# Kernel optimization log

Hardware: AMD Instinct MI355X
Metric: run time of the kernel (lower is better)

## Reference

```python
import jax, jax.numpy as jnp
import numpy as np

N_RBF = 20
CUTOFF = 5.0
N_BASIS = 128
N_FILTERS = 128
N_LAYERS = 3
B, N = 128, 128
N_PAIRS = 524288


def ssp(x):
    # ShiftedSoftplus: softplus(x) - log(2)
    return jax.nn.softplus(x) - jnp.log(2.0).astype(x.dtype)


def gaussian_rbf(d):
    # schnetpack-style GaussianRBF: offsets in [0, cutoff], shared width
    offsets = jnp.linspace(0.0, CUTOFF, N_RBF, dtype=d.dtype)
    width = offsets[1] - offsets[0]
    coeff = -0.5 / (width * width)
    diff = d[:, None] - offsets[None, :]  # [n_pairs, n_rbf]
    return jnp.exp(coeff * diff * diff)


def cosine_cutoff(d):
    fc = 0.5 * (jnp.cos(d * (jnp.pi / CUTOFF)) + 1.0)
    return fc * (d < CUTOFF).astype(d.dtype)


def setup_inputs() -> dict:
    key = jax.random.key(0)
    ks = jax.random.split(key, 16)
    inp = {
        "Z": jax.random.randint(ks[0], (B, N), 0, 100),
        "R": jax.random.normal(ks[1], (B, N, 3), dtype=jnp.float32) * 2.0,
        "idx_i": jax.random.randint(ks[2], (N_PAIRS,), 0, B * N),
        "idx_j": jax.random.randint(ks[3], (N_PAIRS,), 0, B * N),
        "emb": jax.random.normal(ks[4], (100, N_BASIS), dtype=jnp.float32) * 0.1,
    }
    s = 0.05
    inp["in2f_W"] = jax.random.normal(ks[5], (N_LAYERS, N_BASIS, N_FILTERS), dtype=jnp.float32) * s
    inp["in2f_b"] = jnp.zeros((N_LAYERS, N_FILTERS), dtype=jnp.float32)
    inp["fW1"] = jax.random.normal(ks[6], (N_LAYERS, N_RBF, N_FILTERS), dtype=jnp.float32) * s
    inp["fb1"] = jnp.zeros((N_LAYERS, N_FILTERS), dtype=jnp.float32)
    inp["fW2"] = jax.random.normal(ks[7], (N_LAYERS, N_FILTERS, N_FILTERS), dtype=jnp.float32) * s
    inp["fb2"] = jnp.zeros((N_LAYERS, N_FILTERS), dtype=jnp.float32)
    inp["oW1"] = jax.random.normal(ks[8], (N_LAYERS, N_FILTERS, N_BASIS), dtype=jnp.float32) * s
    inp["ob1"] = jnp.zeros((N_LAYERS, N_BASIS), dtype=jnp.float32)
    inp["oW2"] = jax.random.normal(ks[9], (N_LAYERS, N_BASIS, N_BASIS), dtype=jnp.float32) * s
    inp["ob2"] = jnp.zeros((N_LAYERS, N_BASIS), dtype=jnp.float32)
    return inp


def _interaction(x, f_ij, rcut_ij, idx_i, idx_j, W_in, b_in, fW1, fb1, fW2, fb2, oW1, ob1, oW2, ob2):
    # x: [B, N, n_atom_basis]
    h = jnp.einsum("bnf,fg->bng", x, W_in) + b_in          # input_to_feature
    h = h.reshape(-1, h.shape[-1])                           # [B*N, n_filters]
    # filter network on RBFs
    Wij = ssp(f_ij @ fW1 + fb1) @ fW2 + fb2                  # [n_pairs, n_filters]
    Wij = Wij * rcut_ij[:, None]
    x_ij = h[idx_j] * Wij                                     # gather + multiply
    agg = jax.ops.segment_sum(x_ij, idx_i, num_segments=h.shape[0])  # scatter_add
    out = ssp(agg @ oW1 + ob1) @ oW2 + ob2                    # feature_to_output
    return out.reshape(x.shape[0], x.shape[1], N_BASIS)


def reference(Z, R, idx_i, idx_j, emb, in2f_W, in2f_b, fW1, fb1, fW2, fb2, oW1, ob1, oW2, ob2):
    coords = R.reshape(-1, 3)                                 # [B*N, 3]
    vec = coords[idx_i] - coords[idx_j]
    d_ij = jnp.linalg.norm(vec, axis=-1)                      # [n_pairs]
    f_ij = gaussian_rbf(d_ij)                                 # [n_pairs, 20]
    rcut_ij = cosine_cutoff(d_ij)                             # [n_pairs]
    x = emb[Z]                                                # [B, N, 128]
    for l in range(N_LAYERS):
        v = _interaction(x, f_ij, rcut_ij, idx_i, idx_j,
                         in2f_W[l], in2f_b[l], fW1[l], fb1[l], fW2[l], fb2[l],
                         oW1[l], ob1[l], oW2[l], ob2[l])
        x = x + v
    return x
```

## Files before the change

kernel.cpp:

```cpp
#include <hip/hip_runtime.h>
#include <hip/hip_fp16.h>

#define NPAIRS 524288
#define NATOMS 16384
#define TBINS  2048
#define TROWS  2049
#define CAP    80
#define CUTOFF_F 5.0f

#define MB_G0    256
#define MB_TAB   (MB_G0 + 771)
#define MB_WC    (MB_TAB + 72)
#define MB_TOTAL (MB_WC + 2048)

typedef _Float16 f16;
typedef f16 f16x4 __attribute__((ext_vector_type(4)));
typedef f16 f16x8 __attribute__((ext_vector_type(8)));
typedef float f32x4 __attribute__((ext_vector_type(4)));

__device__ __forceinline__ float sspf(float v) {
  float a = fabsf(v);
  return fmaxf(v, 0.0f) + log1pf(expf(-a)) - 0.69314718055994531f;
}

__device__ __forceinline__ int swz(int row, int kh) {
  return (row << 8) + ((kh << 1) ^ ((row & 7) << 4));
}
__device__ __forceinline__ int swzW(int col, int kh) {
  return (col << 7) + ((kh << 1) ^ ((col & 7) << 4));
}
__device__ __forceinline__ f16x8 ldW(const f16* __restrict__ Wg, int col, int ss, int hi) {
  return *(const f16x8*)((const char*)Wg + (ss >> 1) * 16384 + swzW(col, (ss & 1) * 32 + hi * 8));
}

__device__ __forceinline__ uint4 ld16(const char* __restrict__ base, int byteOff) {
  return *(const uint4*)(base + byteOff);
}
__device__ __forceinline__ void dot8(float* acc, uint4 wv, uint4 hv) {
  const __half* wp = (const __half*)&wv;
  const __half* hp = (const __half*)&hv;
  #pragma unroll
  for (int q = 0; q < 8; ++q)
    acc[q] = fmaf(__half2float(wp[q]), __half2float(hp[q]), acc[q]);
}

__global__ __launch_bounds__(256) void zero_kernel(int* __restrict__ p) {
  p[blockIdx.x * 256 + threadIdx.x] = 0;
}

__global__ __launch_bounds__(256) void mega(const int* __restrict__ Z,
                                            const float* __restrict__ emb,
                                            const float* __restrict__ in2f_W,
                                            const float* __restrict__ in2f_b,
                                            const float* __restrict__ fW1,
                                            const float* __restrict__ fb1,
                                            const float* __restrict__ fW2,
                                            const float* __restrict__ fb2,
                                            const float* __restrict__ oW1,
                                            const float* __restrict__ oW2,
                                            const int* __restrict__ idx_i,
                                            const int* __restrict__ idx_j,
                                            const float* __restrict__ R,
                                            f16* __restrict__ table,
                                            f16* __restrict__ wsw,
                                            int* __restrict__ cursor,
                                            int2* __restrict__ pjd,
                                            f16* __restrict__ hout) {
  __shared__ char smem[16384];
  int t = threadIdx.x;
  int bid = blockIdx.x;

  if (bid < MB_G0) {
    char* Wl = smem;
    size_t rbase = (size_t)bid * 64;
    int w = t >> 6, lane = t & 63;
    int lo = lane & 15, hi = lane >> 4;

    int z = Z[rbase + 16 * w + lo];
    const float* erow = emb + (size_t)z * 128;
    f16x8 fa[4];
    #pragma unroll
    for (int ss = 0; ss < 4; ++ss) {
      float4 a = *(const float4*)(erow + ss * 32 + hi * 8);
      float4 b = *(const float4*)(erow + ss * 32 + hi * 8 + 4);
      f16x8 v = { (f16)a.x, (f16)a.y, (f16)a.z, (f16)a.w,
                  (f16)b.x, (f16)b.y, (f16)b.z, (f16)b.w };
      fa[ss] = v;
    }

    f32x4 acc[8];
    #pragma unroll
    for (int cb = 0; cb < 8; ++cb) acc[cb] = (f32x4){0.0f, 0.0f, 0.0f, 0.0f};

    #pragma unroll
    for (int h = 0; h < 2; ++h) {
      #pragma unroll
      for (int i = 0; i < 4; ++i) {
        int tloc = i * 256 + t;
        int col = tloc & 127, kc = tloc >> 7;
        f16x8 v;
        #pragma unroll
        for (int kk = 0; kk < 8; ++kk)
          v[kk] = (f16)in2f_W[(h * 64 + kc * 8 + kk) * 128 + col];
        *(f16x8*)(Wl + swzW(col, kc * 8)) = v;
      }
      __syncthreads();
      #pragma unroll
      for (int cb = 0; cb < 8; ++cb) {
        int col = cb * 16 + lo;
        #pragma unroll
        for (int sh = 0; sh < 2; ++sh) {
          f16x8 fb = *(f16x8*)(Wl + swzW(col, sh * 32 + hi * 8));
          acc[cb] = __builtin_amdgcn_mfma_f32_16x16x32_f16(fa[h * 2 + sh], fb, acc[cb], 0, 0, 0);
        }
      }
      __syncthreads();
    }

    #pragma unroll
    for (int cb = 0; cb < 8; ++cb) {
      int col = cb * 16 + lo;
      float bc = in2f_b[col];
      #pragma unroll
      for (int j = 0; j < 4; ++j)
        hout[(rbase + 16 * w + hi * 4 + j) * 128 + col] = (f16)(acc[cb][j] + bc);
    }
    return;
  }

  if (bid < MB_TAB) {
    float* hid = (float*)smem;
    int bid2 = bid - MB_G0;
    int l = bid2 / 257, rem = bid2 % 257;
    int e = t >> 5, q = t & 31;
    int ti = rem * 8 + e;
    const float* W1 = fW1 + (size_t)l * 20 * 128;
    const float* B1 = fb1 + (size_t)l * 128;
    const float* W2 = fW2 + (size_t)l * 128 * 128;
    const float* B2 = fb2 + (size_t)l * 128;

    const float width = CUTOFF_F / 19.0f;
    const float coeff = -0.5f / (width * width);
    const float dstep = CUTOFF_F / (float)TBINS;
    float d = (float)ti * dstep;

    float4 h4 = *(const float4*)&B1[q * 4];
    #pragma unroll
    for (int r = 0; r < 20; ++r) {
      float diff = d - (float)r * width;
      float fr = expf(coeff * diff * diff);
      float4 w4 = *(const float4*)&W1[r * 128 + q * 4];
      h4.x += fr * w4.x; h4.y += fr * w4.y; h4.z += fr * w4.z; h4.w += fr * w4.w;
    }
    *(float4*)&hid[e * 128 + q * 4] =
        make_float4(sspf(h4.x), sspf(h4.y), sspf(h4.z), sspf(h4.w));
    __syncthreads();

    float4 o4 = *(const float4*)&B2[q * 4];
    const float4* W2g = (const float4*)W2;
    #pragma unroll 4
    for (int g = 0; g < 128; ++g) {
      float hv = hid[e * 128 + g];
      float4 w4 = W2g[g * 32 + q];
      o4.x += hv * w4.x; o4.y += hv * w4.y; o4.z += hv * w4.z; o4.w += hv * w4.w;
    }

    if (ti < TROWS) {
      float fc = (d < CUTOFF_F) ? 0.5f * (cosf(d * 0.62831853071795865f) + 1.0f) : 0.0f;
      f16x4 hv = { (f16)(o4.x * fc), (f16)(o4.y * fc), (f16)(o4.z * fc), (f16)(o4.w * fc) };
      *(f16x4*)((f16*)table + ((size_t)l * TROWS + ti) * 128 + q * 4) = hv;
    }
    return;
  }

  if (bid < MB_WC) {
    int bid2 = bid - MB_TAB;
    int mm = bid2 >> 3;
    int tloc = (bid2 & 7) * 256 + t;
    int col = tloc & 127, k0 = (tloc >> 7) << 3;
    const float* src = mm < 3 ? in2f_W + (size_t)mm * 16384
                     : mm < 6 ? oW1 + (size_t)(mm - 3) * 16384
                              : oW2 + (size_t)(mm - 6) * 16384;
    f16x8 v;
    #pragma unroll
    for (int kk = 0; kk < 8; ++kk) v[kk] = (f16)src[(k0 + kk) * 128 + col];
    *(f16x8*)((char*)wsw + (size_t)mm * 32768 + (k0 >> 6) * 16384 + swzW(col, k0 & 63)) = v;
    return;
  }

  {
    int p = (bid - MB_WC) * 256 + t;
    int i = idx_i[p], j = idx_j[p];
    float dx = R[(size_t)i*3+0] - R[(size_t)j*3+0];
    float dy = R[(size_t)i*3+1] - R[(size_t)j*3+1];
    float dz = R[(size_t)i*3+2] - R[(size_t)j*3+2];
    float d = sqrtf(dx*dx + dy*dy + dz*dz);
    if (d < CUTOFF_F) {
      int bin = __float2int_rn(d * ((float)TBINS / CUTOFF_F));
      int slot = atomicAdd(&cursor[i], 1);
      if (slot < CAP) pjd[i * CAP + slot] = make_int2(j << 8, bin << 8);
    }
  }
}

template <int FIRST, int HAS_NEXT>
__global__ __launch_bounds__(512, 4) void aggfuse(const int2* __restrict__ pjd,
                                                  const int* __restrict__ cnt,
                                                  const f16* __restrict__ hin,
                                                  const f16* __restrict__ tabL,
                                                  const f16* __restrict__ W1g,
                                                  const float* __restrict__ ob1,
                                                  const f16* __restrict__ W2g,
                                                  const float* __restrict__ ob2,
                                                  const int* __restrict__ Z,
                                                  const float* __restrict__ emb,
                                                  float* __restrict__ x,
                                                  const f16* __restrict__ Wng,
                                                  const float* __restrict__ bn,
                                                  f16* __restrict__ hout) {
  __shared__ char smem[8192];
  char* AlT = smem;
  char* Tl  = smem + 4096;
  int tid = threadIdx.x;
  int wv = tid >> 6, lane = tid & 63;
  int s = lane >> 4, c = lane & 15;
  int rbase = blockIdx.x * 16;

  {
    int a = rbase + wv * 2 + (s & 1);
    int half = s >> 1;
    const int2* pp = pjd + a * CAP;
    int n = min(cnt[a], CAP);
    int nh = half * 2;
    const char* hinB = (const char*)hin;
    const char* tabB = (const char*)tabL;
    int cb16 = c << 4;

    int m = (n + 3) >> 2;
    m = max(m, __shfl_xor(m, 16, 64));
    m = max(m, __shfl_xor(m, 32, 64));

    float acc[8];
    #pragma unroll
    for (int q = 0; q < 8; ++q) acc[q] = 0.0f;
    const int2 S2 = make_int2(0, TBINS << 8);

    int2 vA  = (nh     < n) ? pp[nh]     : S2;
    int2 vB  = (nh + 1 < n) ? pp[nh + 1] : S2;
    int2 vA1 = (nh + 4 < n) ? pp[nh + 4] : S2;
    int2 vB1 = (nh + 5 < n) ? pp[nh + 5] : S2;
    uint4 wA = ld16(tabB, vA.y + cb16), hA = ld16(hinB, vA.x + cb16);
    uint4 wB = ld16(tabB, vB.y + cb16), hB = ld16(hinB, vB.x + cb16);

    for (int it = 0; it < m; ++it) {
      int k2 = 4 * (it + 2) + nh;
      int2 vA2 = (k2 < n)     ? pp[k2]     : S2;
      int2 vB2 = (k2 + 1 < n) ? pp[k2 + 1] : S2;
      uint4 wAn = ld16(tabB, vA1.y + cb16), hAn = ld16(hinB, vA1.x + cb16);
      uint4 wBn = ld16(tabB, vB1.y + cb16), hBn = ld16(hinB, vB1.x + cb16);
      dot8(acc, wA, hA);
      dot8(acc, wB, hB);
      wA = wAn; hA = hAn; wB = wBn; hB = hBn;
      vA1 = vA2; vB1 = vB2;
    }

    #pragma unroll
    for (int q = 0; q < 8; ++q) acc[q] += __shfl_xor(acc[q], 32, 64);

    if (s < 2) {
      int row = wv * 2 + s;
      f16x8 pk;
      #pragma unroll
      for (int q = 0; q < 8; ++q) pk[q] = (f16)acc[q];
      *(f16x8*)(AlT + swz(row, c * 8)) = pk;
    }
  }
  __syncthreads();

  int lo = c, hi = s;
  int col = wv * 16 + lo;

  float res[4];
  if (FIRST) {
    #pragma unroll
    for (int j = 0; j < 4; ++j) {
      int z = Z[rbase + hi * 4 + j];
      res[j] = emb[(size_t)z * 128 + col];
    }
  } else {
    #pragma unroll
    for (int j = 0; j < 4; ++j)
      res[j] = x[(size_t)(rbase + hi * 4 + j) * 128 + col];
  }

  {
    f32x4 acc = {0.0f, 0.0f, 0.0f, 0.0f};
    #pragma unroll
    for (int ss = 0; ss < 4; ++ss) {
      f16x8 fa = *(f16x8*)(AlT + swz(lo, ss * 32 + hi * 8));
      acc = __builtin_amdgcn_mfma_f32_16x16x32_f16(fa, ldW(W1g, col, ss, hi), acc, 0, 0, 0);
    }
    float bc = ob1[col];
    #pragma unroll
    for (int j = 0; j < 4; ++j)
      *(f16*)(Tl + swz(hi * 4 + j, col)) = (f16)sspf(acc[j] + bc);
  }
  __syncthreads();

  {
    f32x4 acc = {0.0f, 0.0f, 0.0f, 0.0f};
    #pragma unroll
    for (int ss = 0; ss < 4; ++ss) {
      f16x8 fa = *(f16x8*)(Tl + swz(lo, ss * 32 + hi * 8));
      acc = __builtin_amdgcn_mfma_f32_16x16x32_f16(fa, ldW(W2g, col, ss, hi), acc, 0, 0, 0);
    }
    float bc = ob2[col];
    #pragma unroll
    for (int j = 0; j < 4; ++j) {
      int r = hi * 4 + j;
      float xn = res[j] + acc[j] + bc;
      x[(size_t)(rbase + r) * 128 + col] = xn;
      if (HAS_NEXT) *(f16*)(AlT + swz(r, col)) = (f16)xn;
    }
  }

  if (HAS_NEXT) {
    __syncthreads();
    f32x4 acc = {0.0f, 0.0f, 0.0f, 0.0f};
    #pragma unroll
    for (int ss = 0; ss < 4; ++ss) {
      f16x8 fa = *(f16x8*)(AlT + swz(lo, ss * 32 + hi * 8));
      acc = __builtin_amdgcn_mfma_f32_16x16x32_f16(fa, ldW(Wng, col, ss, hi), acc, 0, 0, 0);
    }
    float bc = bn[col];
    #pragma unroll
    for (int j = 0; j < 4; ++j)
      hout[(size_t)(rbase + hi * 4 + j) * 128 + col] = (f16)(acc[j] + bc);
  }
}

extern "C" void kernel_launch(void* const* d_in, const int* in_sizes, int n_in,
                              void* d_out, int out_size, void* d_ws, size_t ws_size,
                              hipStream_t stream) {
  const int*   Z      = (const int*)d_in[0];
  const float* R      = (const float*)d_in[1];
  const int*   idx_i  = (const int*)d_in[2];
  const int*   idx_j  = (const int*)d_in[3];
  const float* emb    = (const float*)d_in[4];
  const float* in2f_W = (const float*)d_in[5];
  const float* in2f_b = (const float*)d_in[6];
  const float* fW1    = (const float*)d_in[7];
  const float* fb1    = (const float*)d_in[8];
  const float* fW2    = (const float*)d_in[9];
  const float* fb2    = (const float*)d_in[10];
  const float* oW1    = (const float*)d_in[11];
  const float* ob1    = (const float*)d_in[12];
  const float* oW2    = (const float*)d_in[13];
  const float* ob2    = (const float*)d_in[14];
  float* x = (float*)d_out;

  char* ws = (char*)d_ws;
  int*  cursor = (int*) (ws + 0x0000000);
  int2* pjd    = (int2*)(ws + 0x0010000);
  f16*  table  = (f16*) (ws + 0x0B00000);
  f16*  h0     = (f16*) (ws + 0x0D00000);
  f16*  h1     = (f16*) (ws + 0x1100000);
  f16*  wsw    = (f16*) (ws + 0x1500000);

  zero_kernel<<<NATOMS / 256, 256, 0, stream>>>(cursor);
  mega<<<MB_TOTAL, 256, 0, stream>>>(Z, emb, in2f_W, in2f_b, fW1, fb1, fW2, fb2,
                                     oW1, oW2, idx_i, idx_j, R,
                                     table, wsw, cursor, pjd, h0);

  aggfuse<1, 1><<<NATOMS / 16, 512, 0, stream>>>(pjd, cursor, h0, table + 0 * (size_t)TROWS * 128,
                                                 wsw + 3 * 16384, ob1,
                                                 wsw + 6 * 16384, ob2,
                                                 Z, emb, x,
                                                 wsw + 1 * 16384, in2f_b + 128, h1);
  aggfuse<0, 1><<<NATOMS / 16, 512, 0, stream>>>(pjd, cursor, h1, table + 1 * (size_t)TROWS * 128,
                                                 wsw + 4 * 16384, ob1 + 128,
                                                 wsw + 7 * 16384, ob2 + 128,
                                                 Z, emb, x,
                                                 wsw + 2 * 16384, in2f_b + 256, h0);
  aggfuse<0, 0><<<NATOMS / 16, 512, 0, stream>>>(pjd, cursor, h0, table + 2 * (size_t)TROWS * 128,
                                                 wsw + 5 * 16384, ob1 + 256,
                                                 wsw + 8 * 16384, ob2 + 256,
                                                 Z, emb, x, nullptr, nullptr, nullptr);
}
```

Before: 116.4 us.

## Fuse three layer kernels into one persistent kernel with grid barriers

```diff
diff --git a/kernel.cpp b/kernel.cpp
--- a/kernel.cpp
+++ b/kernel.cpp
@@ -7,6 +7,7 @@
 #define TROWS  2049
 #define CAP    80
 #define CUTOFF_F 5.0f
+#define NBLK   512
 
 #define MB_G0    256
 #define MB_TAB   (MB_G0 + 771)
@@ -44,8 +45,10 @@
     acc[q] = fmaf(__half2float(wp[q]), __half2float(hp[q]), acc[q]);
 }
 
-__global__ __launch_bounds__(256) void zero_kernel(int* __restrict__ p) {
-  p[blockIdx.x * 256 + threadIdx.x] = 0;
+__global__ __launch_bounds__(256) void zero_kernel(int* __restrict__ cursor,
+                                                   int* __restrict__ barr) {
+  if (blockIdx.x < NATOMS / 256) cursor[blockIdx.x * 256 + threadIdx.x] = 0;
+  else barr[threadIdx.x] = 0;
 }
 
 __global__ __launch_bounds__(256) void mega(const int* __restrict__ Z,
@@ -203,85 +206,71 @@
   }
 }
 
-template <int FIRST, int HAS_NEXT>
-__global__ __launch_bounds__(512, 4) void aggfuse(const int2* __restrict__ pjd,
-                                                  const int* __restrict__ cnt,
-                                                  const f16* __restrict__ hin,
-                                                  const f16* __restrict__ tabL,
-                                                  const f16* __restrict__ W1g,
-                                                  const float* __restrict__ ob1,
-                                                  const f16* __restrict__ W2g,
-                                                  const float* __restrict__ ob2,
-                                                  const int* __restrict__ Z,
-                                                  const float* __restrict__ emb,
-                                                  float* __restrict__ x,
-                                                  const f16* __restrict__ Wng,
-                                                  const float* __restrict__ bn,
-                                                  f16* __restrict__ hout) {
-  __shared__ char smem[8192];
-  char* AlT = smem;
-  char* Tl  = smem + 4096;
-  int tid = threadIdx.x;
-  int wv = tid >> 6, lane = tid & 63;
-  int s = lane >> 4, c = lane & 15;
-  int rbase = blockIdx.x * 16;
-
-  {
-    int a = rbase + wv * 2 + (s & 1);
-    int half = s >> 1;
-    const int2* pp = pjd + a * CAP;
-    int n = min(cnt[a], CAP);
-    int nh = half * 2;
-    const char* hinB = (const char*)hin;
-    const char* tabB = (const char*)tabL;
-    int cb16 = c << 4;
-
-    int m = (n + 3) >> 2;
-    m = max(m, __shfl_xor(m, 16, 64));
-    m = max(m, __shfl_xor(m, 32, 64));
-
-    float acc[8];
-    #pragma unroll
-    for (int q = 0; q < 8; ++q) acc[q] = 0.0f;
-    const int2 S2 = make_int2(0, TBINS << 8);
-
-    int2 vA  = (nh     < n) ? pp[nh]     : S2;
-    int2 vB  = (nh + 1 < n) ? pp[nh + 1] : S2;
-    int2 vA1 = (nh + 4 < n) ? pp[nh + 4] : S2;
-    int2 vB1 = (nh + 5 < n) ? pp[nh + 5] : S2;
-    uint4 wA = ld16(tabB, vA.y + cb16), hA = ld16(hinB, vA.x + cb16);
-    uint4 wB = ld16(tabB, vB.y + cb16), hB = ld16(hinB, vB.x + cb16);
-
-    for (int it = 0; it < m; ++it) {
-      int k2 = 4 * (it + 2) + nh;
-      int2 vA2 = (k2 < n)     ? pp[k2]     : S2;
-      int2 vB2 = (k2 + 1 < n) ? pp[k2 + 1] : S2;
-      uint4 wAn = ld16(tabB, vA1.y + cb16), hAn = ld16(hinB, vA1.x + cb16);
-      uint4 wBn = ld16(tabB, vB1.y + cb16), hBn = ld16(hinB, vB1.x + cb16);
-      dot8(acc, wA, hA);
-      dot8(acc, wB, hB);
-      wA = wAn; hA = hAn; wB = wBn; hB = hBn;
-      vA1 = vA2; vB1 = vB2;
-    }
-
-    #pragma unroll
-    for (int q = 0; q < 8; ++q) acc[q] += __shfl_xor(acc[q], 32, 64);
-
-    if (s < 2) {
-      int row = wv * 2 + s;
-      f16x8 pk;
-      #pragma unroll
-      for (int q = 0; q < 8; ++q) pk[q] = (f16)acc[q];
-      *(f16x8*)(AlT + swz(row, c * 8)) = pk;
-    }
-  }
-  __syncthreads();
-
-  int lo = c, hi = s;
+__device__ __forceinline__ void agg_tile(int rbase, const int2* __restrict__ pjd,
+                                         const int* __restrict__ cnt,
+                                         const char* __restrict__ hinB,
+                                         const char* __restrict__ tabB,
+                                         char* AlT, int wv, int s, int c) {
+  int a = rbase + wv * 2 + (s & 1);
+  int half = s >> 1;
+  const int2* pp = pjd + a * CAP;
+  int n = min(cnt[a], CAP);
+  int nh = half * 2;
+  int cb16 = c << 4;
+
+  int m = (n + 3) >> 2;
+  m = max(m, __shfl_xor(m, 16, 64));
+  m = max(m, __shfl_xor(m, 32, 64));
+
+  float acc[8];
+  #pragma unroll
+  for (int q = 0; q < 8; ++q) acc[q] = 0.0f;
+  const int2 S2 = make_int2(0, TBINS << 8);
+
+  int2 vA  = (nh     < n) ? pp[nh]     : S2;
+  int2 vB  = (nh + 1 < n) ? pp[nh + 1] : S2;
+  int2 vA1 = (nh + 4 < n) ? pp[nh + 4] : S2;
+  int2 vB1 = (nh + 5 < n) ? pp[nh + 5] : S2;
+  uint4 wA = ld16(tabB, vA.y + cb16), hA = ld16(hinB, vA.x + cb16);
+  uint4 wB = ld16(tabB, vB.y + cb16), hB = ld16(hinB, vB.x + cb16);
+
+  for (int it = 0; it < m; ++it) {
+    int k2 = 4 * (it + 2) + nh;
+    int2 vA2 = (k2 < n)     ? pp[k2]     : S2;
+    int2 vB2 = (k2 + 1 < n) ? pp[k2 + 1] : S2;
+    uint4 wAn = ld16(tabB, vA1.y + cb16), hAn = ld16(hinB, vA1.x + cb16);
+    uint4 wBn = ld16(tabB, vB1.y + cb16), hBn = ld16(hinB, vB1.x + cb16);
+    dot8(acc, wA, hA);
+    dot8(acc, wB, hB);
+    wA = wAn; hA = hAn; wB = wBn; hB = hBn;
+    vA1 = vA2; vB1 = vB2;
+  }
+
+  #pragma unroll
+  for (int q = 0; q < 8; ++q) acc[q] += __shfl_xor(acc[q], 32, 64);
+
+  if (s < 2) {
+    int row = wv * 2 + s;
+    f16x8 pk;
+    #pragma unroll
+    for (int q = 0; q < 8; ++q) pk[q] = (f16)acc[q];
+    *(f16x8*)(AlT + swz(row, c * 8)) = pk;
+  }
+}
+
+__device__ __forceinline__ void fuse_tile(int rbase, char* AlT, char* Tl,
+                                          const f16* __restrict__ W1g, const float* __restrict__ ob1,
+                                          const f16* __restrict__ W2g, const float* __restrict__ ob2,
+                                          bool first, const int* __restrict__ Z,
+                                          const float* __restrict__ emb, float* __restrict__ x,
+                                          bool hasNext, const f16* __restrict__ Wng,
+                                          const float* __restrict__ bn, f16* __restrict__ hout,
+                                          int wv, int lane) {
+  int lo = lane & 15, hi = lane >> 4;
   int col = wv * 16 + lo;
 
   float res[4];
-  if (FIRST) {
+  if (first) {
     #pragma unroll
     for (int j = 0; j < 4; ++j) {
       int z = Z[rbase + hi * 4 + j];
@@ -320,12 +309,12 @@
       int r = hi * 4 + j;
       float xn = res[j] + acc[j] + bc;
       x[(size_t)(rbase + r) * 128 + col] = xn;
-      if (HAS_NEXT) *(f16*)(AlT + swz(r, col)) = (f16)xn;
-    }
-  }
-
-  if (HAS_NEXT) {
-    __syncthreads();
+      if (hasNext) *(f16*)(AlT + swz(r, col)) = (f16)xn;
+    }
+  }
+  __syncthreads();
+
+  if (hasNext) {
     f32x4 acc = {0.0f, 0.0f, 0.0f, 0.0f};
     #pragma unroll
     for (int ss = 0; ss < 4; ++ss) {
@@ -336,6 +325,67 @@
     #pragma unroll
     for (int j = 0; j < 4; ++j)
       hout[(size_t)(rbase + hi * 4 + j) * 128 + col] = (f16)(acc[j] + bc);
+  }
+}
+
+__device__ __forceinline__ void gridbar(int* __restrict__ bar) {
+  __syncthreads();
+  if (threadIdx.x == 0) {
+    __threadfence();
+    atomicAdd(bar, 1);
+    while (atomicAdd(bar, 0) < NBLK) __builtin_amdgcn_s_sleep(2);
+    __threadfence();
+  }
+  __syncthreads();
+}
+
+__global__ __launch_bounds__(512, 4) void aggfuse3(const int2* __restrict__ pjd,
+                                                   const int* __restrict__ cnt,
+                                                   f16* __restrict__ h0,
+                                                   f16* __restrict__ h1,
+                                                   const f16* __restrict__ table,
+                                                   const f16* __restrict__ wsw,
+                                                   const float* __restrict__ in2f_b,
+                                                   const float* __restrict__ ob1,
+                                                   const float* __restrict__ ob2,
+                                                   const int* __restrict__ Z,
+                                                   const float* __restrict__ emb,
+                                                   float* __restrict__ x,
+                                                   int* __restrict__ barr) {
+  __shared__ char smem[12288];
+  char* AlT0 = smem;
+  char* AlT1 = smem + 4096;
+  char* Tl   = smem + 8192;
+  int tid = threadIdx.x;
+  int wv = tid >> 6, lane = tid & 63;
+  int s = lane >> 4, c = lane & 15;
+  int rb0 = blockIdx.x * 16;
+  int rb1 = (blockIdx.x + NBLK) * 16;
+
+  for (int l = 0; l < 3; ++l) {
+    f16* hin  = (l == 1) ? h1 : h0;
+    f16* hout = (l == 0) ? h1 : h0;
+    const char* hinB = (const char*)hin;
+    const char* tabB = (const char*)(table + (size_t)l * TROWS * 128);
+    const f16* W1g = wsw + (size_t)(3 + l) * 16384;
+    const f16* W2g = wsw + (size_t)(6 + l) * 16384;
+    const f16* Wng = wsw + (size_t)(1 + l) * 16384;
+    const float* b1 = ob1 + l * 128;
+    const float* b2 = ob2 + l * 128;
+    const float* bn = in2f_b + (l + 1) * 128;
+    bool first = (l == 0), hasNext = (l < 2);
+
+    agg_tile(rb0, pjd, cnt, hinB, tabB, AlT0, wv, s, c);
+    agg_tile(rb1, pjd, cnt, hinB, tabB, AlT1, wv, s, c);
+    __syncthreads();
+
+    fuse_tile(rb0, AlT0, Tl, W1g, b1, W2g, b2, first, Z, emb, x,
+              hasNext, Wng, bn, hout, wv, lane);
+    __syncthreads();
+    fuse_tile(rb1, AlT1, Tl, W1g, b1, W2g, b2, first, Z, emb, x,
+              hasNext, Wng, bn, hout, wv, lane);
+
+    if (l < 2) gridbar(&barr[l]);
   }
 }
 
@@ -362,28 +412,16 @@
   char* ws = (char*)d_ws;
   int*  cursor = (int*) (ws + 0x0000000);
   int2* pjd    = (int2*)(ws + 0x0010000);
+  int*  barr   = (int*) (ws + 0x0A20000);
   f16*  table  = (f16*) (ws + 0x0B00000);
   f16*  h0     = (f16*) (ws + 0x0D00000);
   f16*  h1     = (f16*) (ws + 0x1100000);
   f16*  wsw    = (f16*) (ws + 0x1500000);
 
-  zero_kernel<<<NATOMS / 256, 256, 0, stream>>>(cursor);
+  zero_kernel<<<NATOMS / 256 + 1, 256, 0, stream>>>(cursor, barr);
   mega<<<MB_TOTAL, 256, 0, stream>>>(Z, emb, in2f_W, in2f_b, fW1, fb1, fW2, fb2,
                                      oW1, oW2, idx_i, idx_j, R,
                                      table, wsw, cursor, pjd, h0);
-
-  aggfuse<1, 1><<<NATOMS / 16, 512, 0, stream>>>(pjd, cursor, h0, table + 0 * (size_t)TROWS * 128,
-                                                 wsw + 3 * 16384, ob1,
-                                                 wsw + 6 * 16384, ob2,
-                                                 Z, emb, x,
-                                                 wsw + 1 * 16384, in2f_b + 128, h1);
-  aggfuse<0, 1><<<NATOMS / 16, 512, 0, stream>>>(pjd, cursor, h1, table + 1 * (size_t)TROWS * 128,
-                                                 wsw + 4 * 16384, ob1 + 128,
-                                                 wsw + 7 * 16384, ob2 + 128,
-                                                 Z, emb, x,
-                                                 wsw + 2 * 16384, in2f_b + 256, h0);
-  aggfuse<0, 0><<<NATOMS / 16, 512, 0, stream>>>(pjd, cursor, h0, table + 2 * (size_t)TROWS * 128,
-                                                 wsw + 5 * 16384, ob1 + 256,
-                                                 wsw + 8 * 16384, ob2 + 256,
-                                                 Z, emb, x, nullptr, nullptr, nullptr);
-}
+  aggfuse3<<<NBLK, 512, 0, stream>>>(pjd, cursor, h0, h1, table, wsw,
+                                     in2f_b, ob1, ob2, Z, emb, x, barr);
+}
```

Result: slower. 265.4 us (+128.0%).
